# Performance work log

Measured on AMD Instinct MI355X. Metric: run time of the kernel, lower is better.

Reference implementation:

```python
import jax, jax.numpy as jnp
import numpy as np

NUM_T = 1000      # diffusion timesteps
TIME_DIM = 16     # gaussian time embedding size
DIST_DIM = 16     # gaussian distance embedding size


def _gsmear(x, stop, num_g):
    # GaussianSmearing with linearly spaced centers in [0, stop]
    offsets = jnp.linspace(0.0, stop, num_g)
    coeff = -0.5 / (offsets[1] - offsets[0]) ** 2
    return jnp.exp(coeff * (x[:, None] - offsets[None, :]) ** 2)


def setup_inputs():
    key = jax.random.key(0)
    ks = jax.random.split(key, 20)
    N, EH, G = 20000, 100000, 1000          # nodes, halfedges, graphs
    NT, ND, ED, L, NE = 16, 256, 128, 2, 5   # node types, node_dim, edge_dim, blocks, edge types
    h_node = jax.nn.one_hot(jax.random.randint(ks[0], (N,), 0, NT), NT, dtype=jnp.float32)
    pos_node = jax.random.normal(ks[1], (N, 3), dtype=jnp.float32) * 3.0
    batch_node = jnp.sort(jax.random.randint(ks[2], (N,), 0, G))
    half = jax.random.randint(ks[3], (2, EH), 0, N)
    edge_index = jnp.concatenate([half, half[::-1]], axis=1)  # halfedges + flipped
    bh = jnp.sort(jax.random.randint(ks[4], (EH,), 0, G))
    batch_edge = jnp.concatenate([bh, bh], axis=0)
    t = jax.random.randint(ks[5], (G,), 0, NUM_T)

    def w(k, shape):
        fan_in = shape[-2] if len(shape) > 1 else shape[-1]
        return jax.random.normal(k, shape, dtype=jnp.float32) / np.sqrt(fan_in)

    e_in = ED + 2 * ND + DIST_DIM + 1
    return {
        'h_node': h_node, 'pos_node': pos_node, 'batch_node': batch_node,
        'edge_index': edge_index, 'batch_edge': batch_edge, 't': t,
        'W_node_emb': w(ks[6], (NT, ND - TIME_DIM)),
        'W_edge_emb': w(ks[7], (2 * NT, ED - TIME_DIM)),
        'We1': w(ks[8], (L, e_in, ED)), 'be1': jnp.zeros((L, ED), jnp.float32),
        'We2': w(ks[9], (L, ED, ED)), 'be2': jnp.zeros((L, ED), jnp.float32),
        'Wm': w(ks[10], (L, ND + ED, ND)), 'bm': jnp.zeros((L, ND), jnp.float32),
        'Wn1': w(ks[11], (L, 2 * ND + 1, ND)), 'bn1': jnp.zeros((L, ND), jnp.float32),
        'Wn2': w(ks[12], (L, ND, ND)), 'bn2': jnp.zeros((L, ND), jnp.float32),
        'Wd1': w(ks[13], (ED + ND, ED)), 'bd1': jnp.zeros((ED,), jnp.float32),
        'Wd2': w(ks[14], (ED, ED)), 'bd2': jnp.zeros((ED,), jnp.float32),
        'Wd3': w(ks[15], (ED, NE)), 'bd3': jnp.zeros((NE,), jnp.float32),
    }


def reference(h_node, pos_node, batch_node, edge_index, batch_edge, t,
              W_node_emb, W_edge_emb, We1, be1, We2, be2, Wm, bm,
              Wn1, bn1, Wn2, bn2, Wd1, bd1, Wd2, bd2, Wd3, bd3):
    src, dst = edge_index[0], edge_index[1]
    N = h_node.shape[0]
    L = We1.shape[0]

    # edge input features: concat of endpoint node features (gather)
    h_e0 = jnp.concatenate([h_node[src], h_node[dst]], axis=-1)

    tn = t[batch_node].astype(jnp.float32)  # per-node timestep
    te = t[batch_edge].astype(jnp.float32)  # per-edge timestep
    # linear embed + gaussian-smeared time embedding
    h_n = jnp.concatenate([h_node @ W_node_emb, _gsmear(tn, float(NUM_T), TIME_DIM)], axis=-1)
    h_e = jnp.concatenate([h_e0 @ W_edge_emb, _gsmear(te, float(NUM_T), TIME_DIM)], axis=-1)
    node_time = (tn / NUM_T)[:, None]
    edge_time = (te / NUM_T)[:, None]

    # geometric edge features
    d = jnp.linalg.norm(pos_node[dst] - pos_node[src], axis=-1)
    dist_emb = _gsmear(d, 10.0, DIST_DIM)

    # NodeEdgeNet: alternating edge / node residual updates
    for l in range(L):
        e_in = jnp.concatenate([h_e, h_n[src], h_n[dst], dist_emb, edge_time], axis=-1)
        h_e = h_e + jax.nn.relu(e_in @ We1[l] + be1[l]) @ We2[l] + be2[l]
        msg = jax.nn.relu(jnp.concatenate([h_n[src], h_e], axis=-1) @ Wm[l] + bm[l])
        agg = jax.ops.segment_sum(msg, dst, num_segments=N)
        n_in = jnp.concatenate([h_n, agg, node_time], axis=-1)
        h_n = h_n + jax.nn.relu(n_in @ Wn1[l] + bn1[l]) @ Wn2[l] + bn2[l]

    # symmetrize halfedges and decode edge types
    nh = h_e.shape[0] // 2
    h_ext = jnp.concatenate([h_e[:nh] + h_e[nh:],
                             h_n[src[:nh]] + h_n[dst[:nh]]], axis=-1)
    h = jax.nn.relu(h_ext @ Wd1 + bd1)
    h = jax.nn.relu(h @ Wd2 + bd2)
    return h @ Wd3 + bd3
```

## Files before the change

### kernel.cpp

```cpp
#include <hip/hip_runtime.h>
#include <math.h>


typedef __attribute__((ext_vector_type(8)))  short bf16x8;
typedef __attribute__((ext_vector_type(16))) float f32x16;

__device__ __forceinline__ float b2f(unsigned short u) {
    union { float f; unsigned int i; } x; x.i = ((unsigned int)u) << 16; return x.f;
}
__device__ __forceinline__ unsigned short f2b(float f) {
    union { float f; unsigned int i; } x; x.f = f;
    unsigned int r = x.i + 0x7fffu + ((x.i >> 16) & 1u);
    return (unsigned short)(r >> 16);
}
__device__ __forceinline__ bf16x8 ld8(const unsigned short* p) { return *(const bf16x8*)p; }
__device__ __forceinline__ bf16x8 zero8() { bf16x8 r = {0,0,0,0,0,0,0,0}; return r; }
__device__ __forceinline__ bf16x8 add8(bf16x8 a, bf16x8 b) {
    bf16x8 r;
#pragma unroll
    for (int j = 0; j < 8; j++) r[j] = (short)f2b(b2f((unsigned short)a[j]) + b2f((unsigned short)b[j]));
    return r;
}

#define MFMA4(ACC, A0, A1, B0, B1)                                                   \
    ACC[0][0] = __builtin_amdgcn_mfma_f32_32x32x16_bf16(A0, B0, ACC[0][0], 0, 0, 0); \
    ACC[0][1] = __builtin_amdgcn_mfma_f32_32x32x16_bf16(A0, B1, ACC[0][1], 0, 0, 0); \
    ACC[1][0] = __builtin_amdgcn_mfma_f32_32x32x16_bf16(A1, B0, ACC[1][0], 0, 0, 0); \
    ACC[1][1] = __builtin_amdgcn_mfma_f32_32x32x16_bf16(A1, B1, ACC[1][1], 0, 0, 0);

#define LANE_SETUP()                                  \
    const int tid  = threadIdx.x;                     \
    const int lane = tid & 63;                        \
    const int wave = tid >> 6;                        \
    const int wm = wave >> 1, wn = wave & 1;          \
    const int l31 = lane & 31, l5 = lane >> 5;        \
    (void)wm; (void)wn; (void)lane;

#define PIPELINE4(NITER, FETCH, ACC)                                  \
    {                                                                 \
        bf16x8 pa0[2], pb0[2], pa1[2], pb1[2], pa2[2], pb2[2];        \
        FETCH(0, pa0, pb0);                                           \
        if (1 < (NITER)) FETCH(1, pa1, pb1);                          \
        _Pragma("unroll")                                             \
        for (int i = 0; i < (NITER); i++) {                           \
            if (i + 2 < (NITER)) FETCH(i + 2, pa2, pb2);              \
            MFMA4(ACC, pa0[0], pa0[1], pb0[0], pb0[1]);               \
            pa0[0] = pa1[0]; pa0[1] = pa1[1];                         \
            pb0[0] = pb1[0]; pb0[1] = pb1[1];                         \
            pa1[0] = pa2[0]; pa1[1] = pa2[1];                         \
            pb1[0] = pb2[0]; pb1[1] = pb2[1];                         \
        }                                                             \
    }

#define PIPELINE2(NITER, FETCH, ACC)                                  \
    {                                                                 \
        bf16x8 pa0, pb0[2], pa1, pb1[2], pa2, pb2[2];                 \
        FETCH(0, pa0, pb0);                                           \
        if (1 < (NITER)) FETCH(1, pa1, pb1);                          \
        _Pragma("unroll")                                             \
        for (int i = 0; i < (NITER); i++) {                           \
            if (i + 2 < (NITER)) FETCH(i + 2, pa2, pb2);              \
            ACC[0] = __builtin_amdgcn_mfma_f32_32x32x16_bf16(pa0, pb0[0], ACC[0], 0, 0, 0); \
            ACC[1] = __builtin_amdgcn_mfma_f32_32x32x16_bf16(pa0, pb0[1], ACC[1], 0, 0, 0); \
            pa0 = pa1; pb0[0] = pb1[0]; pb0[1] = pb1[1];              \
            pa1 = pa2; pb1[0] = pb2[0]; pb1[1] = pb2[1];              \
        }                                                             \
    }

#define STAGED_COMPUTE(As, Bs, ACC)                                         \
    _Pragma("unroll")                                                       \
    for (int s = 0; s < 4; s++) {                                           \
        const int ks  = s * 2 + l5;                                         \
        const int ra0 = wm * 64 + l31, ra1 = ra0 + 32;                      \
        const int ca0 = wn * 64 + l31, ca1 = ca0 + 32;                      \
        bf16x8 a0 = *(const bf16x8*)&As[ra0][ks ^ (ra0 & 7)][0];            \
        bf16x8 a1 = *(const bf16x8*)&As[ra1][ks ^ (ra1 & 7)][0];            \
        bf16x8 b0 = *(const bf16x8*)&Bs[ca0][ks ^ (ca0 & 7)][0];            \
        bf16x8 b1 = *(const bf16x8*)&Bs[ca1][ks ^ (ca1 & 7)][0];            \
        MFMA4(ACC, a0, a1, b0, b1);                                         \
    }

__global__ void zero_i32_k(int* p, int n) {
    int i = blockIdx.x * 256 + threadIdx.x;
    if (i < n) p[i] = 0;
}
__global__ void hist_k(const int* __restrict__ dst, int* __restrict__ cnt, int E) {
    int e = blockIdx.x * 256 + threadIdx.x;
    if (e < E) atomicAdd(&cnt[dst[e]], 1);
}
__global__ __launch_bounds__(256) void scan_k(int* __restrict__ cnt, int N) {
    __shared__ int s[256];
    const int tidx  = threadIdx.x;
    const int chunk = (N + 255) / 256;
    const int lo = tidx * chunk;
    const int hi = (lo + chunk < N) ? lo + chunk : N;
    int sum = 0;
    for (int i = lo; i < hi; i++) sum += cnt[i];
    s[tidx] = sum;
    __syncthreads();
    for (int d = 1; d < 256; d <<= 1) {
        int t = (tidx >= d) ? s[tidx - d] : 0;
        __syncthreads();
        s[tidx] += t;
        __syncthreads();
    }
    int base = s[tidx] - sum;
    for (int i = lo; i < hi; i++) {
        int c = cnt[i];
        cnt[i] = base;
        base += c;
    }
}
__global__ void fill_k(const int* __restrict__ src, const int* __restrict__ dst,
                       const int* __restrict__ batch_edge, int* __restrict__ cur,
                       int* __restrict__ eids, int* __restrict__ pos,
                       int* __restrict__ srcp, int* __restrict__ dstp,
                       int* __restrict__ bep, int E) {
    int e = blockIdx.x * 256 + threadIdx.x;
    if (e < E) {
        int p = atomicAdd(&cur[dst[e]], 1);
        eids[p] = e;
        pos[e]  = p;
        srcp[p] = src[e];
        dstp[p] = dst[e];
        bep[p]  = batch_edge[e];
    }
}
__global__ void pad_k(int* eids, int* srcp, int* dstp, int* bep, int E, int Epad) {
    int i = E + blockIdx.x * 256 + threadIdx.x;
    if (i < Epad) { eids[i] = -1; srcp[i] = 0; dstp[i] = -1; bep[i] = 0; }
}

__global__ void typ_k(const float* __restrict__ h_node, int* __restrict__ typ, int N) {
    int i = blockIdx.x * 256 + threadIdx.x;
    if (i >= N) return;
    int ty = 0;
#pragma unroll
    for (int k = 0; k < 16; k++) if (h_node[i * 16 + k] > 0.5f) ty = k;
    typ[i] = ty;
}

struct TrDesc { const float* W; unsigned short* Wt; int K, N, Kpad; };
struct TrAll  { TrDesc d[12]; };

__global__ __launch_bounds__(256) void tr_all_k(TrAll a) {
    TrDesc t = a.d[blockIdx.y];
    int total = t.N * t.Kpad;
    for (int i = blockIdx.x * 256 + threadIdx.x; i < total; i += gridDim.x * 256) {
        int n = i / t.Kpad, k = i - n * t.Kpad;
        float v = (k < t.K) ? t.W[(size_t)k * t.N + n] : 0.f;
        t.Wt[(size_t)n * t.Kpad + k] = f2b(v);
    }
}

__global__ void embed_node_k(const int* __restrict__ typ,
                             const float* __restrict__ Wn,
                             const int* __restrict__ batch_node,
                             const int* __restrict__ t,
                             unsigned short* __restrict__ h_n, int N) {
    int idx = blockIdx.x * 256 + threadIdx.x;
    if (idx >= N * 32) return;
    int row = idx >> 5, seg = idx & 31;
    bf16x8 v;
    if (seg < 30) {
        const float* w = Wn + (size_t)typ[row] * 240 + seg * 8;
#pragma unroll
        for (int j = 0; j < 8; j++) v[j] = (short)f2b(w[j]);
    } else {
        float x = (float)t[batch_node[row]];
#pragma unroll
        for (int j = 0; j < 8; j++) {
            int col = seg * 8 + j;
            float dx = x - (1000.0f / 15.0f) * (float)(col - 240);
            v[j] = (short)f2b(expf(-1.125e-4f * dx * dx));
        }
    }
    *(bf16x8*)&h_n[(size_t)row * 256 + seg * 8] = v;
}

__global__ void embed_edge_k(const int* __restrict__ typ,
                             const float* __restrict__ We,
                             const int* __restrict__ srcp,
                             const int* __restrict__ dstp,
                             const int* __restrict__ bep,
                             const int* __restrict__ t,
                             unsigned short* __restrict__ h_e, int E) {
    int idx = blockIdx.x * 256 + threadIdx.x;
    if (idx >= E * 16) return;
    int row = idx >> 4, seg = idx & 15;
    bf16x8 v;
    if (seg < 14) {
        int d0 = dstp[row]; if (d0 < 0) d0 = 0;
        const float* ws = We + (size_t)typ[srcp[row]] * 112 + seg * 8;
        const float* wd = We + (size_t)(16 + typ[d0]) * 112 + seg * 8;
#pragma unroll
        for (int j = 0; j < 8; j++) v[j] = (short)f2b(ws[j] + wd[j]);
    } else {
        float x = (float)t[bep[row]];
#pragma unroll
        for (int j = 0; j < 8; j++) {
            int col = seg * 8 + j;
            float dx = x - (1000.0f / 15.0f) * (float)(col - 112);
            v[j] = (short)f2b(expf(-1.125e-4f * dx * dx));
        }
    }
    *(bf16x8*)&h_e[(size_t)row * 128 + seg * 8] = v;
}

__global__ __launch_bounds__(256) void edge_fused_k(
    unsigned short* __restrict__ h_e, const unsigned short* __restrict__ h_n,
    const unsigned short* __restrict__ Wt1, const float* __restrict__ be1,
    const unsigned short* __restrict__ Wt2, const float* __restrict__ be2,
    const float* __restrict__ pos, const int* __restrict__ srcp,
    const int* __restrict__ dstp, const int* __restrict__ t,
    const int* __restrict__ bep, int E)
{
    __shared__ __align__(16) char smem[128 * 136 * 2];
    unsigned short (*As)[8][8] = (unsigned short(*)[8][8])smem;
    unsigned short (*Bs)[8][8] = (unsigned short(*)[8][8])(smem + 16384);
    unsigned short (*H)[136]   = (unsigned short(*)[136])smem;

    LANE_SETUP();
    const int row0 = blockIdx.x * 128;
    const int srow = tid >> 3, sks = tid & 7;
    const int sx   = sks ^ (srow & 7);

    int rge[4], sg[4], dg[4]; bool okr[4];
#pragma unroll
    for (int p = 0; p < 4; p++) {
        int r = row0 + srow + p * 32;
        okr[p] = r < E;
        rge[p] = okr[p] ? r : 0;
        sg[p]  = srcp[rge[p]];
        dg[p]  = dstp[rge[p]]; if (dg[p] < 0) dg[p] = 0;
    }

#define EF_LOADA(KC, A)                                                        \
    {                                                                          \
        const int cg = (KC) * 8 + sks;                                         \
        _Pragma("unroll")                                                      \
        for (int p = 0; p < 4; p++) {                                          \
            bf16x8 v;                                                          \
            if (!okr[p] || cg >= 83) {                                         \
                v = zero8();                                                   \
            } else if (cg < 16) {                                              \
                v = ld8(h_e + (size_t)rge[p] * 128 + (cg << 3));               \
            } else if (cg < 48) {                                              \
                v = ld8(h_n + (size_t)sg[p] * 256 + ((cg - 16) << 3));         \
            } else if (cg < 80) {                                              \
                v = ld8(h_n + (size_t)dg[p] * 256 + ((cg - 48) << 3));         \
            } else if (cg < 82) {                                              \
                float dx = pos[dg[p] * 3 + 0] - pos[sg[p] * 3 + 0];            \
                float dy = pos[dg[p] * 3 + 1] - pos[sg[p] * 3 + 1];            \
                float dz = pos[dg[p] * 3 + 2] - pos[sg[p] * 3 + 2];            \
                float dist = sqrtf(dx * dx + dy * dy + dz * dz);               \
                _Pragma("unroll")                                              \
                for (int j = 0; j < 8; j++) {                                  \
                    float u = dist - (10.0f / 15.0f) * (float)((cg - 80) * 8 + j); \
                    v[j] = (short)f2b(expf(-1.125f * u * u));                  \
                }                                                              \
            } else {                                                           \
                v = zero8();                                                   \
                v[0] = (short)f2b((float)t[bep[rge[p]]] * 1e-3f);              \
            }                                                                  \
            A[p] = v;                                                          \
        }                                                                      \
    }
#define EF_LOADB(KC, B)                                                        \
    {                                                                          \
        const int cg = (KC) * 8 + sks;                                         \
        _Pragma("unroll")                                                      \
        for (int p = 0; p < 4; p++) {                                          \
            int col = srow + p * 32;                                           \
            B[p] = (cg < 84) ? ld8(Wt1 + (size_t)col * 672 + (cg << 3)) : zero8(); \
        }                                                                      \
    }

    f32x16 acc[2][2] = {};
    bf16x8 pA[4], pB[4], qA[4], qB[4];
    EF_LOADA(0, pA); EF_LOADB(0, pB);
    for (int kc = 0; kc < 11; kc++) {
#pragma unroll
        for (int p = 0; p < 4; p++) {
            *(bf16x8*)&As[srow + p * 32][sx][0] = pA[p];
            *(bf16x8*)&Bs[srow + p * 32][sx][0] = pB[p];
        }
        if (kc + 1 < 11) { EF_LOADA(kc + 1, qA); EF_LOADB(kc + 1, qB); }
        __syncthreads();
        STAGED_COMPUTE(As, Bs, acc);
        __syncthreads();
#pragma unroll
        for (int p = 0; p < 4; p++) { pA[p] = qA[p]; pB[p] = qB[p]; }
    }
#undef EF_LOADA
#undef EF_LOADB

#pragma unroll
    for (int mt = 0; mt < 2; mt++)
#pragma unroll
        for (int nt = 0; nt < 2; nt++)
#pragma unroll
            for (int r = 0; r < 16; r++) {
                int lrow = wm * 64 + mt * 32 + (r & 3) + 8 * (r >> 2) + 4 * l5;
                int col  = wn * 64 + nt * 32 + l31;
                float v = acc[mt][nt][r] + be1[col];
                H[lrow][col] = f2b(fmaxf(v, 0.f));
            }
    __syncthreads();

    const unsigned short* W2a = Wt2 + (size_t)(wn * 64 + l31) * 128;
    const unsigned short* W2b = Wt2 + (size_t)(wn * 64 + 32 + l31) * 128;
    f32x16 acc2[2][2] = {};
#define EF2_FETCH(i, A, B)                                          \
    {                                                               \
        const int c = 2 * (i) + l5;                                 \
        A[0] = *(const bf16x8*)&H[wm * 64 + l31][c << 3];           \
        A[1] = *(const bf16x8*)&H[wm * 64 + 32 + l31][c << 3];      \
        B[0] = ld8(W2a + (c << 3));                                 \
        B[1] = ld8(W2b + (c << 3));                                 \
    }
    PIPELINE4(8, EF2_FETCH, acc2)
#undef EF2_FETCH

#pragma unroll
    for (int mt = 0; mt < 2; mt++)
#pragma unroll
        for (int nt = 0; nt < 2; nt++)
#pragma unroll
            for (int r = 0; r < 16; r++) {
                int lrow = wm * 64 + mt * 32 + (r & 3) + 8 * (r >> 2) + 4 * l5;
                int grow = row0 + lrow;
                if (grow >= E) continue;
                int col = wn * 64 + nt * 32 + l31;
                size_t off = (size_t)grow * 128 + col;
                float v = acc2[mt][nt][r] + be2[col] + b2f(h_e[off]);
                h_e[off] = f2b(v);
            }
}

__global__ __launch_bounds__(256) void msg_k(
    const unsigned short* __restrict__ h_e, const unsigned short* __restrict__ h_n,
    const unsigned short* __restrict__ Wtm, const float* __restrict__ bm,
    const int* __restrict__ srcp, const int* __restrict__ dstp,
    float* __restrict__ agg, int E, int nRowTiles)
{
    __shared__ __align__(16) char smem[33024 + 512];
    unsigned short (*As)[8][8] = (unsigned short(*)[8][8])smem;
    unsigned short (*Bs)[8][8] = (unsigned short(*)[8][8])(smem + 16384);
    float (*T)[129] = (float(*)[129])smem;
    int* dstv = (int*)(smem + 33024);

    LANE_SETUP();
    const int b    = blockIdx.x;
    const int rowt = (b >> 4) * 8 + (b & 7);
    const int colh = (b >> 3) & 1;
    if (rowt >= nRowTiles) return;
    const int row0 = rowt * 128;
    const int col0 = colh * 128;

    if (tid < 128) dstv[tid] = dstp[row0 + tid];

    const int srow = tid >> 3, sks = tid & 7;
    const int sx   = sks ^ (srow & 7);

    const unsigned short *hns[4], *hep[4]; bool okr[4];
#pragma unroll
    for (int p = 0; p < 4; p++) {
        int r = row0 + srow + p * 32;
        okr[p] = r < E;
        int rg = okr[p] ? r : 0;
        hns[p] = h_n + (size_t)srcp[rg] * 256;
        hep[p] = h_e + (size_t)rg * 128;
    }

#define MSG_LOADA(KC, A)                                                 \
    {                                                                    \
        const int cg = (KC) * 8 + sks;                                   \
        _Pragma("unroll")                                                \
        for (int p = 0; p < 4; p++) {                                    \
            if (!okr[p])      A[p] = zero8();                            \
            else if (cg < 32) A[p] = ld8(hns[p] + (cg << 3));            \
            else              A[p] = ld8(hep[p] + ((cg - 32) << 3));     \
        }                                                                \
    }
#define MSG_LOADB(KC, B)                                                 \
    {                                                                    \
        const int cg = (KC) * 8 + sks;                                   \
        _Pragma("unroll")                                                \
        for (int p = 0; p < 4; p++) {                                    \
            int col = srow + p * 32;                                     \
            B[p] = ld8(Wtm + (size_t)(col0 + col) * 384 + (cg << 3));    \
        }                                                                \
    }

    f32x16 acc[2][2] = {};
    bf16x8 pA[4], pB[4], qA[4], qB[4];
    MSG_LOADA(0, pA); MSG_LOADB(0, pB);
    for (int kc = 0; kc < 6; kc++) {
#pragma unroll
        for (int p = 0; p < 4; p++) {
            *(bf16x8*)&As[srow + p * 32][sx][0] = pA[p];
            *(bf16x8*)&Bs[srow + p * 32][sx][0] = pB[p];
        }
        if (kc + 1 < 6) { MSG_LOADA(kc + 1, qA); MSG_LOADB(kc + 1, qB); }
        __syncthreads();
        STAGED_COMPUTE(As, Bs, acc);
        __syncthreads();
#pragma unroll
        for (int p = 0; p < 4; p++) { pA[p] = qA[p]; pB[p] = qB[p]; }
    }
#undef MSG_LOADA
#undef MSG_LOADB

    for (int ph = 0; ph < 2; ph++) {
        __syncthreads();
        if (wm == ph) {
#pragma unroll
            for (int mt = 0; mt < 2; mt++)
#pragma unroll
                for (int nt = 0; nt < 2; nt++)
#pragma unroll
                    for (int r = 0; r < 16; r++) {
                        int lrow = mt * 32 + (r & 3) + 8 * (r >> 2) + 4 * l5;
                        int col  = wn * 64 + nt * 32 + l31;
                        T[lrow][col] = acc[mt][nt][r] + bm[col0 + col];
                    }
        }
        __syncthreads();
        const int col = tid & 127, seg = tid >> 7;
        const int gcol = col0 + col;
        float run = 0.f; int prev = -1;
#pragma unroll 4
        for (int i = 0; i < 32; i++) {
            int lr = seg * 32 + i;
            int d  = dstv[ph * 64 + lr];
            float v = fmaxf(T[lr][col], 0.f);
            if (d != prev) {
                if (prev >= 0 && run != 0.f) atomicAdd(&agg[(size_t)prev * 256 + gcol], run);
                run = 0.f; prev = d;
            }
            if (d >= 0) run += v;
        }
        if (prev >= 0 && run != 0.f) atomicAdd(&agg[(size_t)prev * 256 + gcol], run);
    }
}

__global__ __launch_bounds__(256) void nin_k(
    const unsigned short* __restrict__ h_n, const float* __restrict__ agg,
    const unsigned short* __restrict__ Wtn1, const float* __restrict__ bn1,
    const int* __restrict__ batch_node, const int* __restrict__ t,
    unsigned short* __restrict__ Hn, int N)
{
    LANE_SETUP();
    const int row0 = blockIdx.x * 64;
    const int col0 = blockIdx.y * 128;

    int rr = row0 + wm * 32 + l31;
    bool ok = rr < N;
    int r = ok ? rr : 0;
    float timev = (float)t[batch_node[r]] * 1e-3f;
    const unsigned short* hp = h_n + (size_t)r * 256;
    const float*          ap = agg + (size_t)r * 256;

    const unsigned short* Wa = Wtn1 + (size_t)(col0 + wn * 64 + l31) * 544;
    const unsigned short* Wb = Wtn1 + (size_t)(col0 + wn * 64 + 32 + l31) * 544;

    f32x16 acc[2] = {};
#define NIN_FETCH(i, A, B)                                              \
    {                                                                   \
        const int c = 2 * (i) + l5;                                     \
        if (!ok) A = zero8();                                           \
        else if (c < 32) A = ld8(hp + (c << 3));                        \
        else if (c < 64) {                                              \
            const float* q = ap + ((c - 32) << 3);                      \
            bf16x8 v;                                                   \
            _Pragma("unroll")                                           \
            for (int j = 0; j < 8; j++) v[j] = (short)f2b(q[j]);        \
            A = v;                                                      \
        } else if (c == 64) { A = zero8(); A[0] = (short)f2b(timev); }  \
        else A = zero8();                                               \
        B[0] = ld8(Wa + (c << 3));                                      \
        B[1] = ld8(Wb + (c << 3));                                      \
    }
    PIPELINE2(34, NIN_FETCH, acc)
#undef NIN_FETCH

#pragma unroll
    for (int nt = 0; nt < 2; nt++)
#pragma unroll
        for (int r2 = 0; r2 < 16; r2++) {
            int lrow = wm * 32 + (r2 & 3) + 8 * (r2 >> 2) + 4 * l5;
            int grow = row0 + lrow;
            if (grow >= N) continue;
            int col = col0 + wn * 64 + nt * 32 + l31;
            float v = fmaxf(acc[nt][r2] + bn1[col], 0.f);
            Hn[(size_t)grow * 256 + col] = f2b(v);
        }
}

__global__ __launch_bounds__(256) void node_plain_k(
    const unsigned short* __restrict__ Hn, const unsigned short* __restrict__ Wtn2,
    const float* __restrict__ bn2, unsigned short* __restrict__ h_n, int N)
{
    LANE_SETUP();
    const int row0 = blockIdx.x * 64;
    const int col0 = blockIdx.y * 128;

    int rr = row0 + wm * 32 + l31;
    bool ok = rr < N;
    const unsigned short* hp = Hn + (size_t)(ok ? rr : 0) * 256;

    const unsigned short* Wa = Wtn2 + (size_t)(col0 + wn * 64 + l31) * 256;
    const unsigned short* Wb = Wtn2 + (size_t)(col0 + wn * 64 + 32 + l31) * 256;

    f32x16 acc[2] = {};
#define NP_FETCH(i, A, B)                          \
    {                                              \
        const int c = 2 * (i) + l5;                \
        A = ok ? ld8(hp + (c << 3)) : zero8();     \
        B[0] = ld8(Wa + (c << 3));                 \
        B[1] = ld8(Wb + (c << 3));                 \
    }
    PIPELINE2(16, NP_FETCH, acc)
#undef NP_FETCH

#pragma unroll
    for (int nt = 0; nt < 2; nt++)
#pragma unroll
        for (int r2 = 0; r2 < 16; r2++) {
            int lrow = wm * 32 + (r2 & 3) + 8 * (r2 >> 2) + 4 * l5;
            int grow = row0 + lrow;
            if (grow >= N) continue;
            int col = col0 + wn * 64 + nt * 32 + l31;
            size_t off = (size_t)grow * 256 + col;
            float v = acc[nt][r2] + bn2[col] + b2f(h_n[off]);
            h_n[off] = f2b(v);
        }
}

__global__ __launch_bounds__(256) void dec_fused_k(
    const unsigned short* __restrict__ h_e, const unsigned short* __restrict__ h_n,
    const unsigned short* __restrict__ Wtd1, const float* __restrict__ bd1,
    const unsigned short* __restrict__ Wtd2, const float* __restrict__ bd2,
    const float* __restrict__ Wd3, const float* __restrict__ bd3,
    const int* __restrict__ src, const int* __restrict__ dst,
    const int* __restrict__ pos, float* __restrict__ out, int nh)
{
    __shared__ __align__(16) char smem[128 * 136 * 2];
    __shared__ __align__(16) unsigned short H2[128][136];
    unsigned short (*As)[8][8] = (unsigned short(*)[8][8])smem;
    unsigned short (*Bs)[8][8] = (unsigned short(*)[8][8])(smem + 16384);
    unsigned short (*H1)[136]  = (unsigned short(*)[136])smem;

    LANE_SETUP();
    const int row0 = blockIdx.x * 128;
    const int srow = tid >> 3, sks = tid & 7;
    const int sx   = sks ^ (srow & 7);

    const unsigned short *pe1[4], *pe2[4], *pns[4], *pnd[4]; bool okr[4];
#pragma unroll
    for (int p = 0; p < 4; p++) {
        int r = row0 + srow + p * 32;
        okr[p] = r < nh;
        int rg = okr[p] ? r : 0;
        pe1[p] = h_e + (size_t)pos[rg] * 128;
        pe2[p] = h_e + (size_t)pos[rg + nh] * 128;
        pns[p] = h_n + (size_t)src[rg] * 256;
        pnd[p] = h_n + (size_t)dst[rg] * 256;
    }

#define DC_LOADA(KC, A)                                                              \
    {                                                                                \
        const int cg = (KC) * 8 + sks;                                               \
        _Pragma("unroll")                                                            \
        for (int p = 0; p < 4; p++) {                                                \
            if (!okr[p])      A[p] = zero8();                                        \
            else if (cg < 16) A[p] = add8(ld8(pe1[p] + (cg << 3)), ld8(pe2[p] + (cg << 3))); \
            else              A[p] = add8(ld8(pns[p] + ((cg - 16) << 3)), ld8(pnd[p] + ((cg - 16) << 3))); \
        }                                                                            \
    }
#define DC_LOADB(KC, B)                                                              \
    {                                                                                \
        const int cg = (KC) * 8 + sks;                                               \
        _Pragma("unroll")                                                            \
        for (int p = 0; p < 4; p++) {                                                \
            int col = srow + p * 32;                                                 \
            B[p] = ld8(Wtd1 + (size_t)col * 384 + (cg << 3));                        \
        }                                                                            \
    }

    f32x16 acc[2][2] = {};
    bf16x8 pA[4], pB[4], qA[4], qB[4];
    DC_LOADA(0, pA); DC_LOADB(0, pB);
    for (int kc = 0; kc < 6; kc++) {
#pragma unroll
        for (int p = 0; p < 4; p++) {
            *(bf16x8*)&As[srow + p * 32][sx][0] = pA[p];
            *(bf16x8*)&Bs[srow + p * 32][sx][0] = pB[p];
        }
        if (kc + 1 < 6) { DC_LOADA(kc + 1, qA); DC_LOADB(kc + 1, qB); }
        __syncthreads();
        STAGED_COMPUTE(As, Bs, acc);
        __syncthreads();
#pragma unroll
        for (int p = 0; p < 4; p++) { pA[p] = qA[p]; pB[p] = qB[p]; }
    }
#undef DC_LOADA
#undef DC_LOADB

#pragma unroll
    for (int mt = 0; mt < 2; mt++)
#pragma unroll
        for (int nt = 0; nt < 2; nt++)
#pragma unroll
            for (int r = 0; r < 16; r++) {
                int lrow = wm * 64 + mt * 32 + (r & 3) + 8 * (r >> 2) + 4 * l5;
                int col  = wn * 64 + nt * 32 + l31;
                H1[lrow][col] = f2b(fmaxf(acc[mt][nt][r] + bd1[col], 0.f));
            }
    __syncthreads();

    const unsigned short* W2a = Wtd2 + (size_t)(wn * 64 + l31) * 128;
    const unsigned short* W2b = Wtd2 + (size_t)(wn * 64 + 32 + l31) * 128;
    f32x16 acc2[2][2] = {};
#define DC2_FETCH(i, A, B)                                          \
    {                                                               \
        const int c = 2 * (i) + l5;                                 \
        A[0] = *(const bf16x8*)&H1[wm * 64 + l31][c << 3];          \
        A[1] = *(const bf16x8*)&H1[wm * 64 + 32 + l31][c << 3];     \
        B[0] = ld8(W2a + (c << 3));                                 \
        B[1] = ld8(W2b + (c << 3));                                 \
    }
    PIPELINE4(8, DC2_FETCH, acc2)
#undef DC2_FETCH

#pragma unroll
    for (int mt = 0; mt < 2; mt++)
#pragma unroll
        for (int nt = 0; nt < 2; nt++)
#pragma unroll
            for (int r = 0; r < 16; r++) {
                int lrow = wm * 64 + mt * 32 + (r & 3) + 8 * (r >> 2) + 4 * l5;
                int col  = wn * 64 + nt * 32 + l31;
                H2[lrow][col] = f2b(fmaxf(acc2[mt][nt][r] + bd2[col], 0.f));
            }
    __syncthreads();

    if (tid < 128) {
        int grow = row0 + tid;
        if (grow < nh) {
            float a5[5] = {0.f, 0.f, 0.f, 0.f, 0.f};
            for (int ks = 0; ks < 16; ks++) {
                bf16x8 hv = *(const bf16x8*)&H2[tid][ks << 3];
#pragma unroll
                for (int j = 0; j < 8; j++) {
                    float a = b2f((unsigned short)hv[j]);
                    int   k = ks * 8 + j;
#pragma unroll
                    for (int c5 = 0; c5 < 5; c5++) a5[c5] += a * Wd3[k * 5 + c5];
                }
            }
#pragma unroll
            for (int c5 = 0; c5 < 5; c5++) out[(size_t)grow * 5 + c5] = a5[c5] + bd3[c5];
        }
    }
}


__global__ void zero_k(float* p, long n) {
    long i = (long)blockIdx.x * 256 + threadIdx.x;
    if (i < n) p[i] = 0.f;
}


extern "C" void kernel_launch(void* const* d_in, const int* in_sizes, int n_in,
                              void* d_out, int out_size, void* d_ws, size_t ws_size,
                              hipStream_t stream) {
    const float* h_node     = (const float*)d_in[0];
    const float* pos_node   = (const float*)d_in[1];
    const int*   batch_node = (const int*)d_in[2];
    const int*   edge_index = (const int*)d_in[3];
    const int*   batch_edge = (const int*)d_in[4];
    const int*   t          = (const int*)d_in[5];
    const float* W_node_emb = (const float*)d_in[6];
    const float* W_edge_emb = (const float*)d_in[7];
    const float* We1 = (const float*)d_in[8];
    const float* be1 = (const float*)d_in[9];
    const float* We2 = (const float*)d_in[10];
    const float* be2 = (const float*)d_in[11];
    const float* Wm  = (const float*)d_in[12];
    const float* bm  = (const float*)d_in[13];
    const float* Wn1 = (const float*)d_in[14];
    const float* bn1 = (const float*)d_in[15];
    const float* Wn2 = (const float*)d_in[16];
    const float* bn2 = (const float*)d_in[17];
    const float* Wd1 = (const float*)d_in[18];
    const float* bd1 = (const float*)d_in[19];
    const float* Wd2 = (const float*)d_in[20];
    const float* bd2 = (const float*)d_in[21];
    const float* Wd3 = (const float*)d_in[22];
    const float* bd3 = (const float*)d_in[23];

    const int N  = in_sizes[0] / 16;
    const int E  = in_sizes[3] / 2;
    const int nh = E / 2;
    const int* src = edge_index;
    const int* dst = edge_index + E;

    const int gE   = (E + 127) / 128;
    const int gE8  = ((gE + 7) / 8) * 8;
    const int gN64 = (N + 63) / 64;
    const int Epad = gE * 128;

    float* agg  = (float*)d_ws;
    int*   cnt  = (int*)(agg + (size_t)N * 256);
    int*   eids = cnt + N;
    int*   pos  = eids + Epad;
    int*   srcp = pos + Epad;
    int*   dstp = srcp + Epad;
    int*   bep  = dstp + Epad;
    int*   typ  = bep + Epad;
    unsigned short* h_e = (unsigned short*)(typ + N);
    unsigned short* h_n = h_e + (size_t)E * 128;
    unsigned short* Hn  = h_n + (size_t)N * 256;
    unsigned short* Wt1  = Hn + (size_t)N * 256;
    unsigned short* Wt2  = Wt1 + 2 * 128 * 672;
    unsigned short* Wtm  = Wt2 + 2 * 128 * 128;
    unsigned short* Wtn1 = Wtm + 2 * 256 * 384;
    unsigned short* Wtn2 = Wtn1 + 2 * 256 * 544;
    unsigned short* Wtd1 = Wtn2 + 2 * 256 * 256;
    unsigned short* Wtd2 = Wtd1 + 128 * 384;

    zero_i32_k<<<(N + 255) / 256, 256, 0, stream>>>(cnt, N);
    hist_k<<<(E + 255) / 256, 256, 0, stream>>>(dst, cnt, E);
    scan_k<<<1, 256, 0, stream>>>(cnt, N);
    fill_k<<<(E + 255) / 256, 256, 0, stream>>>(src, dst, batch_edge, cnt,
                                                eids, pos, srcp, dstp, bep, E);
    if (Epad > E) pad_k<<<1, 256, 0, stream>>>(eids, srcp, dstp, bep, E, Epad);
    typ_k<<<(N + 255) / 256, 256, 0, stream>>>(h_node, typ, N);

    TrAll ta;
    for (int l = 0; l < 2; l++) {
        ta.d[l * 5 + 0] = { We1 + (size_t)l * 657 * 128, Wt1 + (size_t)l * 128 * 672, 657, 128, 672 };
        ta.d[l * 5 + 1] = { We2 + (size_t)l * 128 * 128, Wt2 + (size_t)l * 128 * 128, 128, 128, 128 };
        ta.d[l * 5 + 2] = { Wm  + (size_t)l * 384 * 256, Wtm + (size_t)l * 256 * 384, 384, 256, 384 };
        ta.d[l * 5 + 3] = { Wn1 + (size_t)l * 513 * 256, Wtn1 + (size_t)l * 256 * 544, 513, 256, 544 };
        ta.d[l * 5 + 4] = { Wn2 + (size_t)l * 256 * 256, Wtn2 + (size_t)l * 256 * 256, 256, 256, 256 };
    }
    ta.d[10] = { Wd1, Wtd1, 384, 128, 384 };
    ta.d[11] = { Wd2, Wtd2, 128, 128, 128 };
    tr_all_k<<<dim3(48, 12), 256, 0, stream>>>(ta);

    embed_node_k<<<(N * 32 + 255) / 256, 256, 0, stream>>>(typ, W_node_emb, batch_node, t, h_n, N);
    embed_edge_k<<<(E * 16 + 255) / 256, 256, 0, stream>>>(typ, W_edge_emb, srcp, dstp, bep, t, h_e, E);

    for (int l = 0; l < 2; l++) {
        edge_fused_k<<<gE, 256, 0, stream>>>(
            h_e, h_n, Wt1 + (size_t)l * 128 * 672, be1 + l * 128,
            Wt2 + (size_t)l * 128 * 128, be2 + l * 128,
            pos_node, srcp, dstp, t, bep, E);

        zero_k<<<(int)(((long)N * 256 + 255) / 256), 256, 0, stream>>>(agg, (long)N * 256);
        msg_k<<<gE8 * 2, 256, 0, stream>>>(
            h_e, h_n, Wtm + (size_t)l * 256 * 384, bm + l * 256, srcp, dstp, agg, E, gE);

        nin_k<<<dim3(gN64, 2), 256, 0, stream>>>(
            h_n, agg, Wtn1 + (size_t)l * 256 * 544, bn1 + l * 256, batch_node, t, Hn, N);

        node_plain_k<<<dim3(gN64, 2), 256, 0, stream>>>(
            Hn, Wtn2 + (size_t)l * 256 * 256, bn2 + l * 256, h_n, N);
    }

    dec_fused_k<<<(nh + 127) / 128, 256, 0, stream>>>(
        h_e, h_n, Wtd1, bd1, Wtd2, bd2, Wd3, bd3, src, dst, pos, (float*)d_out, nh);
}
```

Measured before the change: 866.5 us.

## Precompute per-node projections of h_n for edge MLP first layer

Splits the first edge-MLP matmul so that the h_n[src] and h_n[dst] parts are computed once per node by a new proj_k kernel (N×256 output). The edge kernel then gathers the projected rows and adds them in the epilogue. Its K dimension drops from 672 to 192. This removes the redundant per-edge GEMM over gathered node features (E is about 10x N), in exchange for an extra kernel launch, extra weight-transpose work, and bf16 rounding of the intermediate projections.

After: 834.2 us. -3.7%, faster.

```diff
diff --git a/kernel.cpp b/kernel.cpp
--- a/kernel.cpp
+++ b/kernel.cpp
@@ -141,7 +141,7 @@
 }
 
 struct TrDesc { const float* W; unsigned short* Wt; int K, N, Kpad; };
-struct TrAll  { TrDesc d[12]; };
+struct TrAll  { TrDesc d[14]; };
 
 __global__ __launch_bounds__(256) void tr_all_k(TrAll a) {
     TrDesc t = a.d[blockIdx.y];
@@ -151,6 +151,17 @@
         float v = (k < t.K) ? t.W[(size_t)k * t.N + n] : 0.f;
         t.Wt[(size_t)n * t.Kpad + k] = f2b(v);
     }
+}
+
+__global__ void tr_e1_k(const float* __restrict__ We1, unsigned short* __restrict__ Wt1e) {
+    int idx = blockIdx.x * 256 + threadIdx.x;
+    if (idx >= 128 * 192) return;
+    int c = idx / 192, k = idx - c * 192;
+    float v = 0.f;
+    if (k < 128)      v = We1[(size_t)k * 128 + c];
+    else if (k < 144) v = We1[(size_t)(640 + k - 128) * 128 + c];
+    else if (k == 144) v = We1[(size_t)656 * 128 + c];
+    Wt1e[idx] = f2b(v);
 }
 
 __global__ void embed_node_k(const int* __restrict__ typ,
@@ -207,10 +218,49 @@
     *(bf16x8*)&h_e[(size_t)row * 128 + seg * 8] = v;
 }
 
+__global__ __launch_bounds__(256) void proj_k(
+    const unsigned short* __restrict__ h_n, const unsigned short* __restrict__ Wt,
+    unsigned short* __restrict__ out, int N)
+{
+    LANE_SETUP();
+    const int row0 = blockIdx.x * 64;
+    const int col0 = blockIdx.y * 128;
+
+    int rr = row0 + wm * 32 + l31;
+    bool ok = rr < N;
+    const unsigned short* hp = h_n + (size_t)(ok ? rr : 0) * 256;
+
+    const unsigned short* Wa = Wt + (size_t)(col0 + wn * 64 + l31) * 256;
+    const unsigned short* Wb = Wt + (size_t)(col0 + wn * 64 + 32 + l31) * 256;
+
+    f32x16 acc[2] = {};
+#define PJ_FETCH(i, A, B)                          \
+    {                                              \
+        const int c = 2 * (i) + l5;                \
+        A = ok ? ld8(hp + (c << 3)) : zero8();     \
+        B[0] = ld8(Wa + (c << 3));                 \
+        B[1] = ld8(Wb + (c << 3));                 \
+    }
+    PIPELINE2(16, PJ_FETCH, acc)
+#undef PJ_FETCH
+
+#pragma unroll
+    for (int nt = 0; nt < 2; nt++)
+#pragma unroll
+        for (int r2 = 0; r2 < 16; r2++) {
+            int lrow = wm * 32 + (r2 & 3) + 8 * (r2 >> 2) + 4 * l5;
+            int grow = row0 + lrow;
+            if (grow >= N) continue;
+            int col = col0 + wn * 64 + nt * 32 + l31;
+            out[(size_t)grow * 256 + col] = f2b(acc[nt][r2]);
+        }
+}
+
 __global__ __launch_bounds__(256) void edge_fused_k(
-    unsigned short* __restrict__ h_e, const unsigned short* __restrict__ h_n,
-    const unsigned short* __restrict__ Wt1, const float* __restrict__ be1,
+    unsigned short* __restrict__ h_e,
+    const unsigned short* __restrict__ Wt1e, const float* __restrict__ be1,
     const unsigned short* __restrict__ Wt2, const float* __restrict__ be2,
+    const unsigned short* __restrict__ P12,
     const float* __restrict__ pos, const int* __restrict__ srcp,
     const int* __restrict__ dstp, const int* __restrict__ t,
     const int* __restrict__ bep, int E)
@@ -241,22 +291,18 @@
         _Pragma("unroll")                                                      \
         for (int p = 0; p < 4; p++) {                                          \
             bf16x8 v;                                                          \
-            if (!okr[p] || cg >= 83) {                                         \
+            if (!okr[p] || cg >= 19) {                                         \
                 v = zero8();                                                   \
             } else if (cg < 16) {                                              \
                 v = ld8(h_e + (size_t)rge[p] * 128 + (cg << 3));               \
-            } else if (cg < 48) {                                              \
-                v = ld8(h_n + (size_t)sg[p] * 256 + ((cg - 16) << 3));         \
-            } else if (cg < 80) {                                              \
-                v = ld8(h_n + (size_t)dg[p] * 256 + ((cg - 48) << 3));         \
-            } else if (cg < 82) {                                              \
+            } else if (cg < 18) {                                              \
                 float dx = pos[dg[p] * 3 + 0] - pos[sg[p] * 3 + 0];            \
                 float dy = pos[dg[p] * 3 + 1] - pos[sg[p] * 3 + 1];            \
                 float dz = pos[dg[p] * 3 + 2] - pos[sg[p] * 3 + 2];            \
                 float dist = sqrtf(dx * dx + dy * dy + dz * dz);               \
                 _Pragma("unroll")                                              \
                 for (int j = 0; j < 8; j++) {                                  \
-                    float u = dist - (10.0f / 15.0f) * (float)((cg - 80) * 8 + j); \
+                    float u = dist - (10.0f / 15.0f) * (float)((cg - 16) * 8 + j); \
                     v[j] = (short)f2b(expf(-1.125f * u * u));                  \
                 }                                                              \
             } else {                                                           \
@@ -272,20 +318,20 @@
         _Pragma("unroll")                                                      \
         for (int p = 0; p < 4; p++) {                                          \
             int col = srow + p * 32;                                           \
-            B[p] = (cg < 84) ? ld8(Wt1 + (size_t)col * 672 + (cg << 3)) : zero8(); \
+            B[p] = ld8(Wt1e + (size_t)col * 192 + (cg << 3));                  \
         }                                                                      \
     }
 
     f32x16 acc[2][2] = {};
     bf16x8 pA[4], pB[4], qA[4], qB[4];
     EF_LOADA(0, pA); EF_LOADB(0, pB);
-    for (int kc = 0; kc < 11; kc++) {
+    for (int kc = 0; kc < 3; kc++) {
 #pragma unroll
         for (int p = 0; p < 4; p++) {
             *(bf16x8*)&As[srow + p * 32][sx][0] = pA[p];
             *(bf16x8*)&Bs[srow + p * 32][sx][0] = pB[p];
         }
-        if (kc + 1 < 11) { EF_LOADA(kc + 1, qA); EF_LOADB(kc + 1, qB); }
+        if (kc + 1 < 3) { EF_LOADA(kc + 1, qA); EF_LOADB(kc + 1, qB); }
         __syncthreads();
         STAGED_COMPUTE(As, Bs, acc);
         __syncthreads();
@@ -298,14 +344,22 @@
 #pragma unroll
     for (int mt = 0; mt < 2; mt++)
 #pragma unroll
-        for (int nt = 0; nt < 2; nt++)
-#pragma unroll
-            for (int r = 0; r < 16; r++) {
-                int lrow = wm * 64 + mt * 32 + (r & 3) + 8 * (r >> 2) + 4 * l5;
-                int col  = wn * 64 + nt * 32 + l31;
-                float v = acc[mt][nt][r] + be1[col];
+        for (int r = 0; r < 16; r++) {
+            int lrow = wm * 64 + mt * 32 + (r & 3) + 8 * (r >> 2) + 4 * l5;
+            int grow = row0 + lrow;
+            bool ok = grow < E;
+            int rg = ok ? grow : 0;
+            int s = srcp[rg];
+            int d = dstp[rg]; if (d < 0) d = 0;
+            const unsigned short* p1 = P12 + (size_t)s * 256;
+            const unsigned short* p2 = P12 + (size_t)d * 256 + 128;
+#pragma unroll
+            for (int nt = 0; nt < 2; nt++) {
+                int col = wn * 64 + nt * 32 + l31;
+                float v = acc[mt][nt][r] + be1[col] + b2f(p1[col]) + b2f(p2[col]);
                 H[lrow][col] = f2b(fmaxf(v, 0.f));
             }
+        }
     __syncthreads();
 
     const unsigned short* W2a = Wt2 + (size_t)(wn * 64 + l31) * 128;
@@ -723,13 +777,15 @@
     unsigned short* h_e = (unsigned short*)(typ + N);
     unsigned short* h_n = h_e + (size_t)E * 128;
     unsigned short* Hn  = h_n + (size_t)N * 256;
-    unsigned short* Wt1  = Hn + (size_t)N * 256;
-    unsigned short* Wt2  = Wt1 + 2 * 128 * 672;
+    unsigned short* P12 = Hn + (size_t)N * 256;
+    unsigned short* Wt2  = P12 + (size_t)N * 256;
     unsigned short* Wtm  = Wt2 + 2 * 128 * 128;
     unsigned short* Wtn1 = Wtm + 2 * 256 * 384;
     unsigned short* Wtn2 = Wtn1 + 2 * 256 * 544;
     unsigned short* Wtd1 = Wtn2 + 2 * 256 * 256;
     unsigned short* Wtd2 = Wtd1 + 128 * 384;
+    unsigned short* Wt1e = Wtd2 + 128 * 128;
+    unsigned short* Wp12t = Wt1e + 2 * 128 * 192;
 
     zero_i32_k<<<(N + 255) / 256, 256, 0, stream>>>(cnt, N);
     hist_k<<<(E + 255) / 256, 256, 0, stream>>>(dst, cnt, E);
@@ -741,24 +797,31 @@
 
     TrAll ta;
     for (int l = 0; l < 2; l++) {
-        ta.d[l * 5 + 0] = { We1 + (size_t)l * 657 * 128, Wt1 + (size_t)l * 128 * 672, 657, 128, 672 };
-        ta.d[l * 5 + 1] = { We2 + (size_t)l * 128 * 128, Wt2 + (size_t)l * 128 * 128, 128, 128, 128 };
-        ta.d[l * 5 + 2] = { Wm  + (size_t)l * 384 * 256, Wtm + (size_t)l * 256 * 384, 384, 256, 384 };
-        ta.d[l * 5 + 3] = { Wn1 + (size_t)l * 513 * 256, Wtn1 + (size_t)l * 256 * 544, 513, 256, 544 };
-        ta.d[l * 5 + 4] = { Wn2 + (size_t)l * 256 * 256, Wtn2 + (size_t)l * 256 * 256, 256, 256, 256 };
-    }
-    ta.d[10] = { Wd1, Wtd1, 384, 128, 384 };
-    ta.d[11] = { Wd2, Wtd2, 128, 128, 128 };
-    tr_all_k<<<dim3(48, 12), 256, 0, stream>>>(ta);
+        ta.d[l * 6 + 0] = { We2 + (size_t)l * 128 * 128, Wt2 + (size_t)l * 128 * 128, 128, 128, 128 };
+        ta.d[l * 6 + 1] = { Wm  + (size_t)l * 384 * 256, Wtm + (size_t)l * 256 * 384, 384, 256, 384 };
+        ta.d[l * 6 + 2] = { Wn1 + (size_t)l * 513 * 256, Wtn1 + (size_t)l * 256 * 544, 513, 256, 544 };
+        ta.d[l * 6 + 3] = { Wn2 + (size_t)l * 256 * 256, Wtn2 + (size_t)l * 256 * 256, 256, 256, 256 };
+        ta.d[l * 6 + 4] = { We1 + (size_t)l * 657 * 128 + 128 * 128,
+                            Wp12t + (size_t)l * 256 * 256, 256, 128, 256 };
+        ta.d[l * 6 + 5] = { We1 + (size_t)l * 657 * 128 + 384 * 128,
+                            Wp12t + (size_t)l * 256 * 256 + 128 * 256, 256, 128, 256 };
+    }
+    ta.d[12] = { Wd1, Wtd1, 384, 128, 384 };
+    ta.d[13] = { Wd2, Wtd2, 128, 128, 128 };
+    tr_all_k<<<dim3(48, 14), 256, 0, stream>>>(ta);
+    for (int l = 0; l < 2; l++)
+        tr_e1_k<<<96, 256, 0, stream>>>(We1 + (size_t)l * 657 * 128, Wt1e + (size_t)l * 128 * 192);
 
     embed_node_k<<<(N * 32 + 255) / 256, 256, 0, stream>>>(typ, W_node_emb, batch_node, t, h_n, N);
     embed_edge_k<<<(E * 16 + 255) / 256, 256, 0, stream>>>(typ, W_edge_emb, srcp, dstp, bep, t, h_e, E);
 
     for (int l = 0; l < 2; l++) {
+        proj_k<<<dim3(gN64, 2), 256, 0, stream>>>(h_n, Wp12t + (size_t)l * 256 * 256, P12, N);
+
         edge_fused_k<<<gE, 256, 0, stream>>>(
-            h_e, h_n, Wt1 + (size_t)l * 128 * 672, be1 + l * 128,
+            h_e, Wt1e + (size_t)l * 128 * 192, be1 + l * 128,
             Wt2 + (size_t)l * 128 * 128, be2 + l * 128,
-            pos_node, srcp, dstp, t, bep, E);
+            P12, pos_node, srcp, dstp, t, bep, E);
 
         zero_k<<<(int)(((long)N * 256 + 255) / 256), 256, 0, stream>>>(agg, (long)N * 256);
         msg_k<<<gE8 * 2, 256, 0, stream>>>(
```
